# Optimization experiments

Hardware: AMD Instinct MI355X
Metric: run time of the kernel (lower is better)

The kernel has to match this reference:

```python
import jax, jax.numpy as jnp
import numpy as np


def setup_inputs() -> dict:
    key = jax.random.key(0)
    k1, k2, k3 = jax.random.split(key, 3)
    B, H, L, D = 4, 12, 2048, 768
    return {
        "hidden_states": jax.random.normal(k1, (B, L, D), dtype=jnp.float32),
        "attention_mask": jax.random.normal(k2, (B, 1, 1, L), dtype=jnp.float32),
        "self_attention_scores": jax.random.normal(k3, (B, H, L, L), dtype=jnp.float32),
        "K": 1024,
    }


def reference(hidden_states, attention_mask, self_attention_scores, K):
    # hidden_states: (B, L, D); attention_mask: (B, 1, 1, L) additive mask;
    # self_attention_scores: (B, H, L, L)
    B, L, D = hidden_states.shape
    H = self_attention_scores.shape[1]
    K = min(K, L)

    # masked_attention_scores: mask_f[b,q]*mask_f[b,l] outer product times scores,
    # then mean over heads (H) and mean over query dim (L). Fused via einsum so we
    # never materialize a second (B,H,L,L) tensor.
    mask_f = (attention_mask.reshape(B, L) > -10.0).astype(jnp.float32)  # (B, L)
    importance = jnp.einsum("bhql,bq,bl->bl", self_attention_scores, mask_f, mask_f) / (H * L)

    # force CLS token (index 0) to always be kept
    importance = importance.at[:, 0].set(jnp.inf)

    _, topk_idx = jax.lax.top_k(importance, K)  # (B, K)
    # boolean-mask gather in torch preserves original token order -> sort indices
    sorted_idx = jnp.sort(topk_idx, axis=-1)  # (B, K)

    preserved_tokens = jnp.take_along_axis(hidden_states, sorted_idx[:, :, None], axis=1)  # (B, K, D)
    preserved_attention_mask = jnp.take_along_axis(
        attention_mask.reshape(B, L), sorted_idx, axis=1
    ).reshape(B, 1, 1, K)
    tome_size = jnp.ones((B, K, 1), dtype=jnp.float32)
    return preserved_tokens, preserved_attention_mask, tome_size
```

## Files before the change

### kernel.cpp

```cpp
#include <hip/hip_runtime.h>
#include <hip/hip_bf16.h>

#define BB 4
#define HH 12
#define LL 2048
#define DD 768
#define KK 1024

#define RPC 128
#define CHUNKS ((HH * LL) / RPC)
#define GROUPS 12
#define CPG (CHUNKS / GROUPS)
#define RPI 8

typedef float f32x4 __attribute__((ext_vector_type(4)));

__global__ __launch_bounds__(512) void reduce_kernel(
    const float* __restrict__ scores, const float* __restrict__ amask,
    float* __restrict__ partial)
{
    const int chunk = blockIdx.x;
    const int b     = blockIdx.y;
    const int t     = threadIdx.x;
    const int r0    = chunk * RPC;
    const int q0    = r0 & (LL - 1);

    __shared__ float w_lds[RPC];
    if (t < RPC)
        w_lds[t] = (amask[b * LL + q0 + t] > -10.0f) ? 1.0f : 0.0f;
    __syncthreads();

    double acc[4] = {0, 0, 0, 0};
    const f32x4* rowbase =
        (const f32x4*)(scores + (size_t)(b * HH * LL + r0) * LL);

    for (int rr = 0; rr < RPC; rr += RPI) {
        f32x4 v[RPI];
        #pragma unroll
        for (int k = 0; k < RPI; ++k)
            v[k] = __builtin_nontemporal_load(
                       rowbase + (size_t)(rr + k) * (LL / 4) + t);
        #pragma unroll
        for (int k = 0; k < RPI; ++k) {
            const float w = w_lds[rr + k];
            acc[0] += v[k].x * w; acc[1] += v[k].y * w;
            acc[2] += v[k].z * w; acc[3] += v[k].w * w;
        }
    }

    f32x4 r;
    r.x = (float)acc[0]; r.y = (float)acc[1];
    r.z = (float)acc[2]; r.w = (float)acc[3];
    ((f32x4*)(partial + ((size_t)(b * CHUNKS + chunk)) * LL))[t] = r;
}

__global__ __launch_bounds__(128) void fold1_kernel(
    const float* __restrict__ partial, float* __restrict__ grp)
{
    const int b = blockIdx.z;
    const int g = blockIdx.y;
    const int l = (blockIdx.x << 7) + threadIdx.x;

    const float* p = partial + ((size_t)(b * CHUNKS + g * CPG)) * LL + l;
    float v[CPG];
    #pragma unroll
    for (int c = 0; c < CPG; ++c)
        v[c] = __builtin_nontemporal_load(p + (size_t)c * LL);

    double s = 0.0;
    #pragma unroll
    for (int c = 0; c < CPG; ++c)
        s += v[c];

    grp[((size_t)(b * GROUPS + g)) * LL + l] = (float)s;
}

__device__ __forceinline__ unsigned long long dkey(double v) {
    unsigned long long u = (unsigned long long)__double_as_longlong(v);
    return (u & 0x8000000000000000ULL) ? ~u : (u | 0x8000000000000000ULL);
}

__global__ __launch_bounds__(256) void rank_kernel(
    const float* __restrict__ grp, const float* __restrict__ amask,
    int* __restrict__ rank_out)
{
    const int b = blockIdx.y;
    const int t = threadIdx.x;

    __shared__ unsigned long long keys[LL];
    __shared__ int part[256];

    for (int i = t; i < LL; i += 256) {
        double s = 0.0;
        #pragma unroll
        for (int g = 0; g < GROUPS; ++g)
            s += grp[((size_t)(b * GROUPS + g)) * LL + i];
        const double m = (amask[b * LL + i] > -10.0f) ? 1.0 : 0.0;
        double v = s * m;
        if (i == 0) v = __builtin_inf();
        keys[i] = dkey(v);
    }
    __syncthreads();

    const int e  = (blockIdx.x << 6) + (t & 63);
    const int j0 = (t >> 6) * 512;
    const unsigned long long myk = keys[e];

    int r = 0;
    #pragma unroll 8
    for (int jj = 0; jj < 512; ++jj) {
        const int j = j0 + jj;
        const unsigned long long kj = keys[j];
        r += (kj > myk) || (kj == myk && j < e);
    }
    part[t] = r;
    __syncthreads();

    if (t < 64) {
        int rk = part[t] + part[t + 64] + part[t + 128] + part[t + 192];
        rank_out[b * LL + (blockIdx.x << 6) + t] = rk;
    }
}

__global__ __launch_bounds__(1024) void finalize_kernel(
    const int* __restrict__ rank, const float* __restrict__ amask,
    int* __restrict__ topk_idx, float* __restrict__ out)
{
    const int b    = blockIdx.x;
    const int t    = threadIdx.x;
    const int lane = t & 63;

    __shared__ int cnt[32];
    __shared__ int pre[32];

    bool keep[2]; int lpre[2];
    #pragma unroll
    for (int p = 0; p < 2; ++p) {
        const int i = p * 1024 + t;
        keep[p] = rank[b * LL + i] < KK;
        unsigned long long m = __ballot(keep[p]);
        lpre[p] = __popcll(m & ((1ULL << lane) - 1ULL));
        if (lane == 0) cnt[i >> 6] = __popcll(m);
    }
    __syncthreads();
    if (t == 0) {
        int s = 0;
        for (int c = 0; c < 32; ++c) { pre[c] = s; s += cnt[c]; }
    }
    __syncthreads();

    const size_t tok_sz = (size_t)BB * KK * DD;
    #pragma unroll
    for (int p = 0; p < 2; ++p) {
        const int i = p * 1024 + t;
        if (keep[p]) {
            const int pos = pre[i >> 6] + lpre[p];
            topk_idx[b * KK + pos] = i;
            out[tok_sz + (size_t)b * KK + pos] = amask[b * LL + i];
            out[tok_sz + (size_t)BB * KK + (size_t)b * KK + pos] = 1.0f;
        }
    }
}

__global__ __launch_bounds__(192) void gather_kernel(
    const float* __restrict__ hs, const int* __restrict__ topk_idx,
    float* __restrict__ out)
{
    const int k = blockIdx.x;
    const int b = blockIdx.y;
    const int t = threadIdx.x;
    const int id = topk_idx[b * KK + k];
    const float4* src = (const float4*)(hs + (size_t)(b * LL + id) * DD);
    float4*       dst = (float4*)(out + (size_t)(b * KK + k) * DD);
    dst[t] = src[t];
}

extern "C" void kernel_launch(void* const* d_in, const int* in_sizes, int n_in,
                              void* d_out, int out_size, void* d_ws, size_t ws_size,
                              hipStream_t stream) {
    const float* hs     = (const float*)d_in[0];
    const float* amask  = (const float*)d_in[1];
    const float* scores = (const float*)d_in[2];
    float* out = (float*)d_out;

    char* ws = (char*)d_ws;
    float* partial = (float*)ws;
    float* grp  = (float*)(ws + (size_t)BB * CHUNKS * LL * sizeof(float));
    int*   rank = (int*)((char*)grp + (size_t)BB * GROUPS * LL * sizeof(float));
    int*   topk = (int*)((char*)rank + (size_t)BB * LL * sizeof(int));

    reduce_kernel<<<dim3(CHUNKS, BB), 512, 0, stream>>>(scores, amask, partial);
    fold1_kernel<<<dim3(LL / 128, GROUPS, BB), 128, 0, stream>>>(partial, grp);
    rank_kernel<<<dim3(LL / 64, BB), 256, 0, stream>>>(grp, amask, rank);
    finalize_kernel<<<BB, 1024, 0, stream>>>(rank, amask, topk, out);
    gather_kernel<<<dim3(KK, BB), 192, 0, stream>>>(hs, topk, out);
}
```

Baseline: 153.0 us.

## Fuse finalize into rank and gather kernels, dropping a launch

Removes the single-block-per-batch finalize kernel. The rank kernel now emits per-64-token keep counts via a ballot. Each gather block then recomputes its source token index with a prefix sum over those counts and a wavefront ballot, and writes the mask and size outputs itself. This cuts one serialized launch and its low-parallelism tail, at the cost of redundant prefix and rank reads in every gather block plus an extra syncthreads before the copy.

```diff
diff --git a/kernel.cpp b/kernel.cpp
--- a/kernel.cpp
+++ b/kernel.cpp
@@ -82,7 +82,7 @@
 
 __global__ __launch_bounds__(256) void rank_kernel(
     const float* __restrict__ grp, const float* __restrict__ amask,
-    int* __restrict__ rank_out)
+    int* __restrict__ rank_out, int* __restrict__ cnt_out)
 {
     const int b = blockIdx.y;
     const int t = threadIdx.x;
@@ -117,62 +117,61 @@
     __syncthreads();
 
     if (t < 64) {
-        int rk = part[t] + part[t + 64] + part[t + 128] + part[t + 192];
+        const int rk = part[t] + part[t + 64] + part[t + 128] + part[t + 192];
         rank_out[b * LL + (blockIdx.x << 6) + t] = rk;
-    }
-}
-
-__global__ __launch_bounds__(1024) void finalize_kernel(
-    const int* __restrict__ rank, const float* __restrict__ amask,
-    int* __restrict__ topk_idx, float* __restrict__ out)
-{
-    const int b    = blockIdx.x;
-    const int t    = threadIdx.x;
-    const int lane = t & 63;
-
-    __shared__ int cnt[32];
-    __shared__ int pre[32];
-
-    bool keep[2]; int lpre[2];
-    #pragma unroll
-    for (int p = 0; p < 2; ++p) {
-        const int i = p * 1024 + t;
-        keep[p] = rank[b * LL + i] < KK;
-        unsigned long long m = __ballot(keep[p]);
-        lpre[p] = __popcll(m & ((1ULL << lane) - 1ULL));
-        if (lane == 0) cnt[i >> 6] = __popcll(m);
-    }
-    __syncthreads();
-    if (t == 0) {
-        int s = 0;
-        for (int c = 0; c < 32; ++c) { pre[c] = s; s += cnt[c]; }
-    }
-    __syncthreads();
-
-    const size_t tok_sz = (size_t)BB * KK * DD;
-    #pragma unroll
-    for (int p = 0; p < 2; ++p) {
-        const int i = p * 1024 + t;
-        if (keep[p]) {
-            const int pos = pre[i >> 6] + lpre[p];
-            topk_idx[b * KK + pos] = i;
-            out[tok_sz + (size_t)b * KK + pos] = amask[b * LL + i];
-            out[tok_sz + (size_t)BB * KK + (size_t)b * KK + pos] = 1.0f;
-        }
+        const unsigned long long m = __ballot(rk < KK);
+        if (t == 0) cnt_out[b * (LL / 64) + blockIdx.x] = __popcll(m);
     }
 }
 
 __global__ __launch_bounds__(192) void gather_kernel(
-    const float* __restrict__ hs, const int* __restrict__ topk_idx,
+    const float* __restrict__ hs, const int* __restrict__ rank,
+    const int* __restrict__ cnt, const float* __restrict__ amask,
     float* __restrict__ out)
 {
     const int k = blockIdx.x;
     const int b = blockIdx.y;
     const int t = threadIdx.x;
-    const int id = topk_idx[b * KK + k];
-    const float4* src = (const float4*)(hs + (size_t)(b * LL + id) * DD);
-    float4*       dst = (float4*)(out + (size_t)(b * KK + k) * DD);
-    dst[t] = src[t];
+
+    __shared__ int s_cnt[LL / 64];
+    __shared__ int s_id;
+
+    if (t < LL / 64)
+        s_cnt[t] = cnt[b * (LL / 64) + t];
+    __syncthreads();
+
+    if (t < 64) {
+        int g = -1, base = 0;
+        if (t < LL / 64) {
+            int P = 0;
+            #pragma unroll
+            for (int j = 0; j < LL / 64; ++j)
+                P += (j < t) ? s_cnt[j] : 0;
+            if (P <= k && k < P + s_cnt[t]) { g = t; base = P; }
+        }
+        const unsigned long long gm = __ballot(g >= 0);
+        const int src = __ffsll((long long)gm) - 1;
+        g    = __shfl(g, src);
+        base = __shfl(base, src);
+
+        const int rk   = rank[b * LL + (g << 6) + t];
+        const bool kp  = rk < KK;
+        const unsigned long long m = __ballot(kp);
+        const int pw = __popcll(m & ((1ULL << t) - 1ULL));
+        if (kp && pw == k - base) s_id = (g << 6) + t;
+    }
+    __syncthreads();
+
+    const int id = s_id;
+    const float4* src4 = (const float4*)(hs + (size_t)(b * LL + id) * DD);
+    float4*       dst4 = (float4*)(out + (size_t)(b * KK + k) * DD);
+    dst4[t] = src4[t];
+
+    if (t == 0) {
+        const size_t tok_sz = (size_t)BB * KK * DD;
+        out[tok_sz + (size_t)b * KK + k] = amask[b * LL + id];
+        out[tok_sz + (size_t)BB * KK + (size_t)b * KK + k] = 1.0f;
+    }
 }
 
 extern "C" void kernel_launch(void* const* d_in, const int* in_sizes, int n_in,
@@ -187,11 +186,10 @@
     float* partial = (float*)ws;
     float* grp  = (float*)(ws + (size_t)BB * CHUNKS * LL * sizeof(float));
     int*   rank = (int*)((char*)grp + (size_t)BB * GROUPS * LL * sizeof(float));
-    int*   topk = (int*)((char*)rank + (size_t)BB * LL * sizeof(int));
+    int*   cnt  = (int*)((char*)rank + (size_t)BB * LL * sizeof(int));
 
     reduce_kernel<<<dim3(CHUNKS, BB), 512, 0, stream>>>(scores, amask, partial);
     fold1_kernel<<<dim3(LL / 128, GROUPS, BB), 128, 0, stream>>>(partial, grp);
-    rank_kernel<<<dim3(LL / 64, BB), 256, 0, stream>>>(grp, amask, rank);
-    finalize_kernel<<<BB, 1024, 0, stream>>>(rank, amask, topk, out);
-    gather_kernel<<<dim3(KK, BB), 192, 0, stream>>>(hs, topk, out);
+    rank_kernel<<<dim3(LL / 64, BB), 256, 0, stream>>>(grp, amask, rank, cnt);
+    gather_kernel<<<dim3(KK, BB), 192, 0, stream>>>(hs, rank, cnt, amask, out);
 }
```

Result: no change. 152.4 us (-0.4%).
